# Performance work log

Hardware: AMD Instinct MI355X
Metric: run time of the kernel (lower is better)

## Reference

```python
import jax, jax.numpy as jnp
import numpy as np

WIN = 7                      # window_size[0] == window_size[1]
N_TOK = WIN * WIN            # 49 tokens per window
PRETRAIN = 12                # pretrain_window_size
LOG8 = float(np.log(8.0))


def _relative_position_index():
    # tf.meshgrid default 'xy' indexing == np.meshgrid default
    gh, gw = np.meshgrid(np.arange(WIN), np.arange(WIN))
    coords = np.stack([gh, gw], 0).reshape(2, -1)            # [2, N]
    rel = coords[:, :, None] - coords[:, None, :]            # [2, N, N]
    rel = rel.transpose(1, 2, 0)                             # [N, N, 2]
    ry = (rel[..., 0] + WIN - 1) * (2 * WIN - 1)
    rx = rel[..., 1] + WIN - 1
    return jnp.asarray((ry + rx).reshape(-1), dtype=jnp.int32)   # [N*N]


def _relative_coords_table():
    ch = np.arange(-(WIN - 1), WIN, dtype=np.float32)
    gh, gw = np.meshgrid(ch, ch)                             # 'xy' indexing
    t = np.stack([gh, gw], axis=-1)[None]                    # [1, 2W-1, 2W-1, 2]
    t = t / (PRETRAIN - 1)                                   # first divide
    t = t * (8.0 / (PRETRAIN - 1))                           # scale (as in source)
    t = np.sign(t) * np.log1p(np.abs(t)) / LOG8
    return jnp.asarray(t, dtype=jnp.float32)


REL_IDX = _relative_position_index()
COORDS_TABLE = _relative_coords_table()


def _l2_normalize(t, eps=1e-12):
    return t * jax.lax.rsqrt(jnp.maximum(jnp.sum(t * t, axis=-1, keepdims=True), eps))


def setup_inputs() -> dict:
    key = jax.random.key(0)
    ks = jax.random.split(key, 12)
    Bw, N, C, H, RPE_H = 2048, N_TOK, 512, 16, 512
    s = 0.02
    return {
        "x": jax.random.normal(ks[0], (Bw, N, C), jnp.float32),
        "mask": jax.random.normal(ks[1], (64, N, N), jnp.float32),
        "qkv_w": jax.random.normal(ks[2], (C, 3 * C), jnp.float32) * s,
        "q_bias": jnp.zeros((C,), jnp.float32),
        "v_bias": jnp.zeros((C,), jnp.float32),
        "logit_scale": jnp.full((H, 1, 1), np.log(10.0), jnp.float32),
        "rpe_w1": jax.random.normal(ks[3], (2, RPE_H), jnp.float32) * s,
        "rpe_b1": jnp.zeros((RPE_H,), jnp.float32),
        "rpe_w2": jax.random.normal(ks[4], (RPE_H, H), jnp.float32) * s,
        "proj_w": jax.random.normal(ks[5], (C, C), jnp.float32) * s,
        "proj_b": jnp.zeros((C,), jnp.float32),
    }


def reference(x, mask, qkv_w, q_bias, v_bias, logit_scale,
              rpe_w1, rpe_b1, rpe_w2, proj_w, proj_b):
    Bw, N, C = x.shape
    H = logit_scale.shape[0]
    hd = C // H

    qkv_bias = jnp.concatenate([q_bias, jnp.zeros_like(v_bias), v_bias])
    qkv = x @ qkv_w + qkv_bias                          # [Bw, N, 3C]
    qkv = qkv.reshape(Bw, N, 3, H, hd).transpose(2, 0, 3, 1, 4)
    q, k, v = qkv[0], qkv[1], qkv[2]                    # [Bw, H, N, hd]

    scale = jnp.exp(jnp.minimum(logit_scale, jnp.log(1.0 / 0.01)))  # [H,1,1]
    q = _l2_normalize(q)
    k = _l2_normalize(k)
    attn = jnp.einsum('bhnd,bhmd->bhnm', q, k) * scale  # [Bw, H, N, N]

    # RPE MLP on the (2W-1)^2 coords table, then gather per token pair
    h1 = jax.nn.relu(COORDS_TABLE @ rpe_w1 + rpe_b1)
    bias_table = (h1 @ rpe_w2).reshape(-1, H)           # [(2W-1)^2, H]
    pb = bias_table[REL_IDX].reshape(N, N, H).transpose(2, 0, 1)  # [H, N, N]
    attn = attn + 16.0 * jax.nn.sigmoid(pb)[None]

    nW = mask.shape[0]
    attn = attn.reshape(Bw // nW, nW, H, N, N) + mask[None, :, None]
    attn = attn.reshape(Bw, H, N, N)

    attn = jax.nn.softmax(attn, axis=-1)
    out = jnp.einsum('bhnm,bhmd->bnhd', attn, v).reshape(Bw, N, C)
    return out @ proj_w + proj_b
```

## Files before the change

### kernel.cpp

```cpp
#include <hip/hip_runtime.h>
#include <cstdint>

#define NTOK 49
#define CDIM 512
#define BW 2048
#define MROWS (BW * NTOK)
#define QKVN 1536

typedef __attribute__((ext_vector_type(4))) float f32x4;
typedef __attribute__((ext_vector_type(8))) short s16x8;
typedef __attribute__((ext_vector_type(4))) unsigned int u32x4;
typedef __attribute__((ext_vector_type(2))) unsigned int u32x2;

__device__ __forceinline__ uint16_t f2b(float f) {
  uint32_t u = __float_as_uint(f);
  u += 0x7fffu + ((u >> 16) & 1u);
  return (uint16_t)(u >> 16);
}
__device__ __forceinline__ float b2f(uint16_t h) {
  return __uint_as_float(((uint32_t)h) << 16);
}

#define GLOAD_LDS16(gp, lp)                                                    \
  __builtin_amdgcn_global_load_lds(                                            \
      (__attribute__((address_space(1))) void*)(gp),                           \
      (__attribute__((address_space(3))) void*)(lp), 16, 0, 0)

__global__ __launch_bounds__(256) void cvt_x_kernel(const float* __restrict__ x,
                                                    uint16_t* __restrict__ xb) {
  long i = ((long)blockIdx.x * 256 + threadIdx.x) * 4;
  f32x4 v = *(const f32x4*)(x + i);
  uint64_t p = (uint64_t)f2b(v[0]) | ((uint64_t)f2b(v[1]) << 16) |
               ((uint64_t)f2b(v[2]) << 32) | ((uint64_t)f2b(v[3]) << 48);
  *(uint64_t*)(xb + i) = p;
}

__global__ __launch_bounds__(256) void prep_weights(
    const float* __restrict__ qkv_w, const float* __restrict__ proj_w,
    const float* __restrict__ q_bias, const float* __restrict__ v_bias,
    uint16_t* __restrict__ qkv_wT, uint16_t* __restrict__ proj_wT,
    float* __restrict__ qkv_bias) {
  int i = blockIdx.x * 256 + threadIdx.x;
  if (i < QKVN * CDIM) {
    int nn = i / CDIM, kk = i % CDIM;
    qkv_wT[i] = f2b(qkv_w[(long)kk * QKVN + nn]);
  }
  if (i < CDIM * CDIM) {
    int nn = i / CDIM, kk = i % CDIM;
    proj_wT[i] = f2b(proj_w[(long)kk * CDIM + nn]);
  }
  if (i < QKVN) {
    float bv = (i < 512) ? q_bias[i] : (i < 1024 ? 0.f : v_bias[i - 1024]);
    qkv_bias[i] = bv;
  }
}

__global__ __launch_bounds__(256) void rpe_table(const float* __restrict__ w1,
                                                 const float* __restrict__ b1,
                                                 const float* __restrict__ w2,
                                                 float* __restrict__ bias16) {
  int i = blockIdx.x * 256 + threadIdx.x;
  if (i >= 169 * 16) return;
  int f = i >> 4, h = i & 15;
  float d0 = (float)((f % 13) - 6);
  float d1 = (float)((f / 13) - 6);
  const float inv_log8 = 0.4808983469629878f;
  float v0 = (d0 / 11.0f) * (8.0f / 11.0f);
  float v1 = (d1 / 11.0f) * (8.0f / 11.0f);
  float f0 = copysignf(log1pf(fabsf(v0)) * inv_log8, v0);
  if (v0 == 0.f) f0 = 0.f;
  float f1 = copysignf(log1pf(fabsf(v1)) * inv_log8, v1);
  if (v1 == 0.f) f1 = 0.f;
  float acc = 0.f;
  for (int k = 0; k < 512; ++k) {
    float h1 = fmaxf(f0 * w1[k] + f1 * w1[512 + k] + b1[k], 0.f);
    acc += h1 * w2[k * 16 + h];
  }
  bias16[i] = 16.f / (1.f + expf(-acc));
}

__global__ __launch_bounds__(256) void build_tiles(
    const float* __restrict__ mask, const float* __restrict__ bias16,
    float* __restrict__ mask_t, float* __restrict__ bias_t) {
  int bid = blockIdx.x;
  int l = threadIdx.x >> 2, j = threadIdx.x & 3;
  int gg = l >> 4, cc = l & 15;
  if (bid < 1024) {
    int w = bid >> 4, tile = bid & 15;
    int mt = tile >> 2, nt = tile & 3;
    int q = nt * 16 + cc, k = mt * 16 + gg * 4 + j;
    float v;
    if (k >= 49) v = -1e30f;
    else if (q >= 49) v = 0.f;
    else v = mask[(long)w * 2401 + q * 49 + k];
    mask_t[(long)bid * 256 + threadIdx.x] = v;
  } else {
    int idx = bid - 1024;
    int h = idx >> 4, tile = idx & 15;
    int mt = tile >> 2, nt = tile & 3;
    int q = nt * 16 + cc, k = mt * 16 + gg * 4 + j;
    float v = 0.f;
    if (q < 49 && k < 49) {
      int ridx = (q % 7 - k % 7 + 6) * 13 + (q / 7 - k / 7 + 6);
      v = bias16[ridx * 16 + h];
    }
    bias_t[(long)idx * 256 + threadIdx.x] = v;
  }
}


#define STAGE_A(tile, half, buf)                                               \
  {                                                                            \
    const uint16_t* s_ = srcA + (half) * (128L * 512) + (long)(tile) * 64;     \
    uint16_t* d_ = &lds[(buf) * 32768 + (half) * 8192 + tid * 8];              \
    GLOAD_LDS16(s_, d_);                                                       \
    GLOAD_LDS16(s_ + 64 * 512, d_ + 4096);                                     \
  }

#define STAGE_B(tile, half, buf)                                               \
  {                                                                            \
    const uint16_t* s_ = srcB + (half) * (128L * 512) + (long)(tile) * 64;     \
    uint16_t* d_ = &lds[(buf) * 32768 + 16384 + (half) * 8192 + tid * 8];      \
    GLOAD_LDS16(s_, d_);                                                       \
    GLOAD_LDS16(s_ + 64 * 512, d_ + 4096);                                     \
  }

#define VM4 asm volatile("s_waitcnt vmcnt(4)" ::: "memory");
#define VM0 asm volatile("s_waitcnt vmcnt(0)" ::: "memory");

#define PHASE(buf, q, STAGES, TAIL)                                            \
  {                                                                            \
    s16x8 a00 = *(const s16x8*)&lds[(buf)*32768 + arow + (2*(q))*1024 + ax0];  \
    s16x8 a01 = *(const s16x8*)&lds[(buf)*32768 + arow + (2*(q))*1024 + ax1];  \
    s16x8 a10 = *(const s16x8*)&lds[(buf)*32768 + arow + (2*(q)+1)*1024 + ax0];\
    s16x8 a11 = *(const s16x8*)&lds[(buf)*32768 + arow + (2*(q)+1)*1024 + ax1];\
    if ((q) == 0) {                                                            \
      _Pragma("unroll")                                                        \
      for (int nf = 0; nf < 4; ++nf) {                                         \
        bfr0[nf] = *(const s16x8*)&lds[(buf)*32768 + brow_ + nf*1024 + ax0];   \
        bfr1[nf] = *(const s16x8*)&lds[(buf)*32768 + brow_ + nf*1024 + ax1];   \
      }                                                                        \
    }                                                                          \
    STAGES                                                                     \
    __builtin_amdgcn_s_barrier();                                              \
    asm volatile("s_waitcnt lgkmcnt(0)" ::: "memory");                         \
    __builtin_amdgcn_sched_barrier(0);                                         \
    __builtin_amdgcn_s_setprio(1);                                             \
    _Pragma("unroll")                                                          \
    for (int nf = 0; nf < 4; ++nf) {                                           \
      acc[2*(q)][nf] = __builtin_amdgcn_mfma_f32_16x16x32_bf16(                \
          a00, bfr0[nf], acc[2*(q)][nf], 0, 0, 0);                             \
      acc[2*(q)][nf] = __builtin_amdgcn_mfma_f32_16x16x32_bf16(                \
          a01, bfr1[nf], acc[2*(q)][nf], 0, 0, 0);                             \
      acc[2*(q)+1][nf] = __builtin_amdgcn_mfma_f32_16x16x32_bf16(              \
          a10, bfr0[nf], acc[2*(q)+1][nf], 0, 0, 0);                           \
      acc[2*(q)+1][nf] = __builtin_amdgcn_mfma_f32_16x16x32_bf16(              \
          a11, bfr1[nf], acc[2*(q)+1][nf], 0, 0, 0);                           \
    }                                                                          \
    __builtin_amdgcn_s_setprio(0);                                             \
    TAIL                                                                       \
    __builtin_amdgcn_s_barrier();                                              \
  }

template <int EPI>
__global__ __launch_bounds__(512, 2) void gemm8p(const uint16_t* __restrict__ A,
                                                 const uint16_t* __restrict__ BT,
                                                 const float* __restrict__ bias,
                                                 void* __restrict__ Cout,
                                                 int N, int ntn) {
  __shared__ uint16_t lds[2 * 32768];
  const int tid = threadIdx.x;
  const int wave = tid >> 6, lane = tid & 63;
  const int wm = wave >> 2, wn = wave & 3;
  const int c = lane & 15, g = lane >> 4;

  const int bid = blockIdx.x;
  const int nwg = gridDim.x;
  const int wg = (bid & 7) * (nwg >> 3) + (bid >> 3);
  const int mt = wg / ntn, nt = wg % ntn;
  const long brow = (long)mt * 256;
  const int bcol = nt * 256;

  const int lr0 = tid >> 3;
  const int chunk = tid & 7;
  const int scol = (chunk ^ (lr0 & 7)) * 8;
  const uint16_t* srcA = A + (brow + lr0) * 512 + scol;
  const uint16_t* srcB = BT + ((long)bcol + lr0) * 512 + scol;

  const int arow = wm * 8192 + c * 64;
  const int brow_ = 16384 + (wn >> 1) * 8192 + ((wn & 1) * 64 + c) * 64;
  const int ax0 = (g * 8) ^ ((c & 7) * 8);
  const int ax1 = (32 + g * 8) ^ ((c & 7) * 8);

  f32x4 acc[8][4];
#pragma unroll
  for (int i = 0; i < 8; ++i)
#pragma unroll
    for (int j = 0; j < 4; ++j) acc[i][j] = f32x4{0.f, 0.f, 0.f, 0.f};
  s16x8 bfr0[4], bfr1[4];

  STAGE_A(0, 0, 0); STAGE_A(0, 1, 0);
  STAGE_B(0, 0, 0); STAGE_B(0, 1, 0);
  STAGE_B(1, 0, 1); STAGE_B(1, 1, 1);
  asm volatile("s_waitcnt vmcnt(4)" ::: "memory");
  __builtin_amdgcn_s_barrier();

  for (int i = 0; i < 3; ++i) {
    const int t0 = 2 * i;
    PHASE(0, 0, STAGE_A(t0 + 1, 0, 1), )
    PHASE(0, 1, STAGE_A(t0 + 1, 1, 1), )
    PHASE(0, 2, STAGE_B(t0 + 2, 0, 0), )
    PHASE(0, 3, STAGE_B(t0 + 2, 1, 0), VM4)
    PHASE(1, 0, STAGE_A(t0 + 2, 0, 0), )
    PHASE(1, 1, STAGE_A(t0 + 2, 1, 0), )
    PHASE(1, 2, STAGE_B(t0 + 3, 0, 1), )
    PHASE(1, 3, STAGE_B(t0 + 3, 1, 1), VM4)
  }
  PHASE(0, 0, STAGE_A(7, 0, 1), )
  PHASE(0, 1, STAGE_A(7, 1, 1), )
  PHASE(0, 2, , )
  PHASE(0, 3, , VM0)
  PHASE(1, 0, , )
  PHASE(1, 1, , )
  PHASE(1, 2, , )
  PHASE(1, 3, , )

#pragma unroll
  for (int mf = 0; mf < 8; ++mf) {
#pragma unroll
    for (int nf = 0; nf < 4; ++nf) {
      const int col = bcol + wn * 64 + nf * 16 + c;
      const float bv = bias[col];
#pragma unroll
      for (int r = 0; r < 4; ++r) {
        const long grow = brow + wm * 128 + mf * 16 + g * 4 + r;
        const float v = acc[mf][nf][r] + bv;
        if (EPI == 0)
          ((uint16_t*)Cout)[grow * N + col] = f2b(v);
        else
          ((float*)Cout)[grow * N + col] = v;
      }
    }
  }
}

__global__ __launch_bounds__(256, 4) void attn_mfma(
    const uint16_t* __restrict__ qkv,
    const float* __restrict__ logit_scale,
    const float* __restrict__ bias_t,
    const float* __restrict__ mask_t,
    uint16_t* __restrict__ outb) {
  __shared__ uint16_t Vs[4][2048];
  const int tid = threadIdx.x;
  const int wave = tid >> 6, lane = tid & 63;
  const int g = lane >> 4, c = lane & 15;
  const int b = blockIdx.x >> 2;
  const int h = ((blockIdx.x & 3) << 2) | wave;
  const long rbase = (long)b * 49;

  uint16_t* vdst = Vs[wave];
#pragma unroll
  for (int i = 0; i < 4; ++i) {
    int chunk = i * 64 + lane;
    int row = chunk >> 2, part = chunk & 3;
    if (row > 48) { row = 0; part = 0; }
    GLOAD_LDS16(qkv + (rbase + row) * QKVN + 1024 + h * 32 + part * 8,
                vdst + i * 512 + lane * 8);
  }

  const long qoff = rbase * QKVN + h * 32;
  s16x8 kf[4], qf[4];
#pragma unroll
  for (int t = 0; t < 4; ++t) {
    int row = t * 16 + c;
    s16x8 kv = {}, qv = {};
    if (row < 49) {
      qv = *(const s16x8*)(qkv + qoff + (long)row * QKVN + g * 8);
      kv = *(const s16x8*)(qkv + qoff + (long)row * QKVN + 512 + g * 8);
    }
    float kfv[8], qfv[8];
    float kss = 0.f, qss = 0.f;
#pragma unroll
    for (int m = 0; m < 8; ++m) {
      kfv[m] = b2f((uint16_t)kv[m]); kss += kfv[m] * kfv[m];
      qfv[m] = b2f((uint16_t)qv[m]); qss += qfv[m] * qfv[m];
    }
    kss += __shfl_xor(kss, 16); kss += __shfl_xor(kss, 32);
    qss += __shfl_xor(qss, 16); qss += __shfl_xor(qss, 32);
    float kr = rsqrtf(fmaxf(kss, 1e-12f));
    float qr = rsqrtf(fmaxf(qss, 1e-12f));
#pragma unroll
    for (int m = 0; m < 8; ++m) {
      kv[m] = (short)f2b(kfv[m] * kr);
      qv[m] = (short)f2b(qfv[m] * qr);
    }
    kf[t] = kv; qf[t] = qv;
  }

  const float scale = __expf(fminf(logit_scale[h], 4.6051702f));
  const float* bt = bias_t + (long)h * 4096;
  const float* mk = mask_t + (long)(b & 63) * 4096;

  u32x4 aT[4][2];
  const int dstlo = (c + 16 * (g >> 1)) * 4;
  const int dsthi = (c + 16 * (2 + (g >> 1))) * 4;
  const bool godd = (g & 1) != 0;
  const bool low = (lane < 32);

#pragma unroll
  for (int nt = 0; nt < 4; ++nt) {
    f32x4 eb[4], em[4];
#pragma unroll
    for (int mt = 0; mt < 4; ++mt) {
      int tile = mt * 4 + nt;
      eb[mt] = *(const f32x4*)(bt + tile * 256 + lane * 4);
      em[mt] = *(const f32x4*)(mk + tile * 256 + lane * 4);
    }
    f32x4 sv[4];
    __builtin_amdgcn_s_setprio(1);
#pragma unroll
    for (int mt = 0; mt < 4; ++mt)
      sv[mt] = __builtin_amdgcn_mfma_f32_16x16x32_bf16(
          kf[mt], qf[nt], f32x4{0.f, 0.f, 0.f, 0.f}, 0, 0, 0);
    __builtin_amdgcn_s_setprio(0);
#pragma unroll
    for (int mt = 0; mt < 4; ++mt)
#pragma unroll
      for (int j = 0; j < 4; ++j)
        sv[mt][j] = sv[mt][j] * scale + eb[mt][j] + em[mt][j];

    float mx = -3.0e38f;
#pragma unroll
    for (int mt = 0; mt < 4; ++mt)
#pragma unroll
      for (int j = 0; j < 4; ++j) mx = fmaxf(mx, sv[mt][j]);
    mx = fmaxf(mx, __shfl_xor(mx, 16));
    mx = fmaxf(mx, __shfl_xor(mx, 32));
    float sum = 0.f;
#pragma unroll
    for (int mt = 0; mt < 4; ++mt)
#pragma unroll
      for (int j = 0; j < 4; ++j) {
        float e = __expf(sv[mt][j] - mx);
        sv[mt][j] = e; sum += e;
      }
    sum += __shfl_xor(sum, 16);
    sum += __shfl_xor(sum, 32);
    float inv = 1.0f / sum;
#pragma unroll
    for (int mt = 0; mt < 4; ++mt)
#pragma unroll
      for (int j = 0; j < 4; ++j) sv[mt][j] *= inv;

    unsigned pk[4][2];
#pragma unroll
    for (int mt = 0; mt < 4; ++mt) {
      pk[mt][0] = (unsigned)f2b(sv[mt][0]) | ((unsigned)f2b(sv[mt][1]) << 16);
      pk[mt][1] = (unsigned)f2b(sv[mt][2]) | ((unsigned)f2b(sv[mt][3]) << 16);
    }
#pragma unroll
    for (int x = 0; x < 2; ++x)
#pragma unroll
      for (int K = 0; K < 2; ++K) {
        int vA = godd ? (int)pk[2 * K + 1][x] : (int)pk[2 * K][x];
        int dA = godd ? dsthi : dstlo;
        int rA = __builtin_amdgcn_ds_permute(dA, vA);
        int vB = godd ? (int)pk[2 * K][x] : (int)pk[2 * K + 1][x];
        int dB = godd ? dstlo : dsthi;
        int rB = __builtin_amdgcn_ds_permute(dB, vB);
        aT[nt][K][x]     = (unsigned)(low ? rA : rB);
        aT[nt][K][2 + x] = (unsigned)(low ? rB : rA);
      }
  }

  asm volatile("s_waitcnt vmcnt(0)" ::: "memory");

  f32x4 o[4][2];
#pragma unroll
  for (int qt = 0; qt < 4; ++qt)
#pragma unroll
    for (int dt = 0; dt < 2; ++dt) o[qt][dt] = f32x4{0.f, 0.f, 0.f, 0.f};

#pragma unroll
  for (int ks = 0; ks < 2; ++ks) {
    s16x8 vf[2];
#pragma unroll
    for (int dt = 0; dt < 2; ++dt) {
      int d = dt * 16 + c;
      s16x8 vv;
#pragma unroll
      for (int jj = 0; jj < 8; ++jj) {
        int k = ks * 32 + g * 8 + jj;
        vv[jj] = (short)vdst[k * 32 + d];
      }
      vf[dt] = vv;
    }
    __builtin_amdgcn_s_setprio(1);
#pragma unroll
    for (int qt = 0; qt < 4; ++qt) {
      s16x8 pf = __builtin_bit_cast(s16x8, aT[qt][ks]);
#pragma unroll
      for (int dt = 0; dt < 2; ++dt)
        o[qt][dt] = __builtin_amdgcn_mfma_f32_16x16x32_bf16(pf, vf[dt],
                                                            o[qt][dt], 0, 0, 0);
    }
    __builtin_amdgcn_s_setprio(0);
  }

#pragma unroll
  for (int qt = 0; qt < 4; ++qt) {
    int q0 = qt * 16 + g * 4;
#pragma unroll
    for (int dt = 0; dt < 2; ++dt) {
      int d = dt * 16 + c;
#pragma unroll
      for (int j = 0; j < 4; ++j) {
        int q = q0 + j;
        if (q < 49)
          outb[(rbase + q) * 512 + h * 32 + d] = f2b(o[qt][dt][j]);
      }
    }
  }
}

extern "C" void kernel_launch(void* const* d_in, const int* in_sizes, int n_in,
                              void* d_out, int out_size, void* d_ws,
                              size_t ws_size, hipStream_t stream) {
  const float* x = (const float*)d_in[0];
  const float* mask = (const float*)d_in[1];
  const float* qkv_w = (const float*)d_in[2];
  const float* q_bias = (const float*)d_in[3];
  const float* v_bias = (const float*)d_in[4];
  const float* logit_scale = (const float*)d_in[5];
  const float* rpe_w1 = (const float*)d_in[6];
  const float* rpe_b1 = (const float*)d_in[7];
  const float* rpe_w2 = (const float*)d_in[8];
  const float* proj_w = (const float*)d_in[9];
  const float* proj_b = (const float*)d_in[10];

  char* ws = (char*)d_ws;
  uint16_t* xb       = (uint16_t*)ws;
  uint16_t* qkvbuf   = (uint16_t*)(ws + 102760448L);
  uint16_t* qkv_wT   = (uint16_t*)(ws + 411041792L);
  uint16_t* proj_wT  = (uint16_t*)(ws + 412614656L);
  float*    qkv_bias = (float*)(ws + 413138944L);
  float*    bias16   = (float*)(ws + 413145088L);
  float*    bias_t   = (float*)(ws + 413155904L);
  float*    mask_t   = (float*)(ws + 413418048L);

  cvt_x_kernel<<<50176, 256, 0, stream>>>(x, xb);
  prep_weights<<<3072, 256, 0, stream>>>(qkv_w, proj_w, q_bias, v_bias, qkv_wT,
                                         proj_wT, qkv_bias);
  rpe_table<<<11, 256, 0, stream>>>(rpe_w1, rpe_b1, rpe_w2, bias16);
  build_tiles<<<1280, 256, 0, stream>>>(mask, bias16, mask_t, bias_t);

  gemm8p<0><<<2352, 512, 0, stream>>>(xb, qkv_wT, qkv_bias, qkvbuf, QKVN, 6);
  attn_mfma<<<8192, 256, 0, stream>>>(qkvbuf, logit_scale, bias_t, mask_t, xb);
  gemm8p<1><<<784, 512, 0, stream>>>(xb, proj_wT, proj_b, d_out, CDIM, 2);
}
```

Before: 562.0 us.

## Fuse prep kernels and interleave PV MFMA with software-pipelined bias loads

Merges the x conversion, weight transpose and RPE table kernels into a single launch, which removes two kernel launches. In the attention kernel, V fragments are loaded up front and the PV MFMAs run inside the per-query-tile loop, so the full transposed probability array no longer has to stay live. Bias and mask tiles for the next query tile are prefetched while the current one is processed. Separately, the QKV GEMM is split into two half-sized launches, which adds launch overhead without an obvious gain, and the extra prefetch registers may offset the register savings.

```diff
diff --git a/kernel.cpp b/kernel.cpp
--- a/kernel.cpp
+++ b/kernel.cpp
@@ -26,57 +26,55 @@
       (__attribute__((address_space(1))) void*)(gp),                           \
       (__attribute__((address_space(3))) void*)(lp), 16, 0, 0)
 
-__global__ __launch_bounds__(256) void cvt_x_kernel(const float* __restrict__ x,
-                                                    uint16_t* __restrict__ xb) {
-  long i = ((long)blockIdx.x * 256 + threadIdx.x) * 4;
-  f32x4 v = *(const f32x4*)(x + i);
-  uint64_t p = (uint64_t)f2b(v[0]) | ((uint64_t)f2b(v[1]) << 16) |
-               ((uint64_t)f2b(v[2]) << 32) | ((uint64_t)f2b(v[3]) << 48);
-  *(uint64_t*)(xb + i) = p;
-}
-
-__global__ __launch_bounds__(256) void prep_weights(
+__global__ __launch_bounds__(256) void prep_all(
+    const float* __restrict__ x, uint16_t* __restrict__ xb,
     const float* __restrict__ qkv_w, const float* __restrict__ proj_w,
     const float* __restrict__ q_bias, const float* __restrict__ v_bias,
     uint16_t* __restrict__ qkv_wT, uint16_t* __restrict__ proj_wT,
-    float* __restrict__ qkv_bias) {
-  int i = blockIdx.x * 256 + threadIdx.x;
-  if (i < QKVN * CDIM) {
-    int nn = i / CDIM, kk = i % CDIM;
-    qkv_wT[i] = f2b(qkv_w[(long)kk * QKVN + nn]);
-  }
-  if (i < CDIM * CDIM) {
-    int nn = i / CDIM, kk = i % CDIM;
-    proj_wT[i] = f2b(proj_w[(long)kk * CDIM + nn]);
-  }
-  if (i < QKVN) {
-    float bv = (i < 512) ? q_bias[i] : (i < 1024 ? 0.f : v_bias[i - 1024]);
-    qkv_bias[i] = bv;
-  }
-}
-
-__global__ __launch_bounds__(256) void rpe_table(const float* __restrict__ w1,
-                                                 const float* __restrict__ b1,
-                                                 const float* __restrict__ w2,
-                                                 float* __restrict__ bias16) {
-  int i = blockIdx.x * 256 + threadIdx.x;
-  if (i >= 169 * 16) return;
-  int f = i >> 4, h = i & 15;
-  float d0 = (float)((f % 13) - 6);
-  float d1 = (float)((f / 13) - 6);
-  const float inv_log8 = 0.4808983469629878f;
-  float v0 = (d0 / 11.0f) * (8.0f / 11.0f);
-  float v1 = (d1 / 11.0f) * (8.0f / 11.0f);
-  float f0 = copysignf(log1pf(fabsf(v0)) * inv_log8, v0);
-  if (v0 == 0.f) f0 = 0.f;
-  float f1 = copysignf(log1pf(fabsf(v1)) * inv_log8, v1);
-  if (v1 == 0.f) f1 = 0.f;
-  float acc = 0.f;
-  for (int k = 0; k < 512; ++k) {
-    float h1 = fmaxf(f0 * w1[k] + f1 * w1[512 + k] + b1[k], 0.f);
-    acc += h1 * w2[k * 16 + h];
-  }
-  bias16[i] = 16.f / (1.f + expf(-acc));
+    float* __restrict__ qkv_bias, const float* __restrict__ w1,
+    const float* __restrict__ b1, const float* __restrict__ w2,
+    float* __restrict__ bias16) {
+  const int bid = blockIdx.x;
+  if (bid < 50176) {
+    long i = ((long)bid * 256 + threadIdx.x) * 4;
+    f32x4 v = *(const f32x4*)(x + i);
+    uint64_t p = (uint64_t)f2b(v[0]) | ((uint64_t)f2b(v[1]) << 16) |
+                 ((uint64_t)f2b(v[2]) << 32) | ((uint64_t)f2b(v[3]) << 48);
+    *(uint64_t*)(xb + i) = p;
+  } else if (bid < 50176 + 3072) {
+    int i = (bid - 50176) * 256 + threadIdx.x;
+    if (i < QKVN * CDIM) {
+      int nn = i / CDIM, kk = i % CDIM;
+      qkv_wT[i] = f2b(qkv_w[(long)kk * QKVN + nn]);
+    }
+    if (i < CDIM * CDIM) {
+      int nn = i / CDIM, kk = i % CDIM;
+      proj_wT[i] = f2b(proj_w[(long)kk * CDIM + nn]);
+    }
+    if (i < QKVN) {
+      float bv = (i < 512) ? q_bias[i] : (i < 1024 ? 0.f : v_bias[i - 1024]);
+      qkv_bias[i] = bv;
+    }
+  } else {
+    int i = (bid - 53248) * 256 + threadIdx.x;
+    if (i >= 169 * 16) return;
+    int f = i >> 4, h = i & 15;
+    float d0 = (float)((f % 13) - 6);
+    float d1 = (float)((f / 13) - 6);
+    const float inv_log8 = 0.4808983469629878f;
+    float v0 = (d0 / 11.0f) * (8.0f / 11.0f);
+    float v1 = (d1 / 11.0f) * (8.0f / 11.0f);
+    float f0 = copysignf(log1pf(fabsf(v0)) * inv_log8, v0);
+    if (v0 == 0.f) f0 = 0.f;
+    float f1 = copysignf(log1pf(fabsf(v1)) * inv_log8, v1);
+    if (v1 == 0.f) f1 = 0.f;
+    float acc = 0.f;
+    for (int k = 0; k < 512; ++k) {
+      float h1 = fmaxf(f0 * w1[k] + f1 * w1[512 + k] + b1[k], 0.f);
+      acc += h1 * w2[k * 16 + h];
+    }
+    bias16[i] = 16.f / (1.f + expf(-acc));
+  }
 }
 
 __global__ __launch_bounds__(256) void build_tiles(
@@ -297,25 +295,46 @@
     kf[t] = kv; qf[t] = qv;
   }
 
+  asm volatile("s_waitcnt vmcnt(0)" ::: "memory");
+  s16x8 vf[2][2];
+#pragma unroll
+  for (int ks = 0; ks < 2; ++ks)
+#pragma unroll
+    for (int dt = 0; dt < 2; ++dt) {
+      int d = dt * 16 + c;
+      s16x8 vv;
+#pragma unroll
+      for (int jj = 0; jj < 8; ++jj) {
+        int k = ks * 32 + g * 8 + jj;
+        vv[jj] = (short)vdst[k * 32 + d];
+      }
+      vf[ks][dt] = vv;
+    }
+
   const float scale = __expf(fminf(logit_scale[h], 4.6051702f));
   const float* bt = bias_t + (long)h * 4096;
   const float* mk = mask_t + (long)(b & 63) * 4096;
 
-  u32x4 aT[4][2];
   const int dstlo = (c + 16 * (g >> 1)) * 4;
   const int dsthi = (c + 16 * (2 + (g >> 1))) * 4;
   const bool godd = (g & 1) != 0;
   const bool low = (lane < 32);
 
+  f32x4 cbA[4], cmA[4];
+#pragma unroll
+  for (int mt = 0; mt < 4; ++mt) {
+    cbA[mt] = *(const f32x4*)(bt + (mt * 4 + 0) * 256 + lane * 4);
+    cmA[mt] = *(const f32x4*)(mk + (mt * 4 + 0) * 256 + lane * 4);
+  }
+
+  f32x4 o[4][2];
+#pragma unroll
+  for (int qt = 0; qt < 4; ++qt)
+#pragma unroll
+    for (int dt = 0; dt < 2; ++dt) o[qt][dt] = f32x4{0.f, 0.f, 0.f, 0.f};
+
 #pragma unroll
   for (int nt = 0; nt < 4; ++nt) {
-    f32x4 eb[4], em[4];
-#pragma unroll
-    for (int mt = 0; mt < 4; ++mt) {
-      int tile = mt * 4 + nt;
-      eb[mt] = *(const f32x4*)(bt + tile * 256 + lane * 4);
-      em[mt] = *(const f32x4*)(mk + tile * 256 + lane * 4);
-    }
     f32x4 sv[4];
     __builtin_amdgcn_s_setprio(1);
 #pragma unroll
@@ -323,11 +342,21 @@
       sv[mt] = __builtin_amdgcn_mfma_f32_16x16x32_bf16(
           kf[mt], qf[nt], f32x4{0.f, 0.f, 0.f, 0.f}, 0, 0, 0);
     __builtin_amdgcn_s_setprio(0);
+
+    f32x4 cbN[4], cmN[4];
+    if (nt < 3) {
+#pragma unroll
+      for (int mt = 0; mt < 4; ++mt) {
+        cbN[mt] = *(const f32x4*)(bt + (mt * 4 + nt + 1) * 256 + lane * 4);
+        cmN[mt] = *(const f32x4*)(mk + (mt * 4 + nt + 1) * 256 + lane * 4);
+      }
+    }
+
 #pragma unroll
     for (int mt = 0; mt < 4; ++mt)
 #pragma unroll
       for (int j = 0; j < 4; ++j)
-        sv[mt][j] = sv[mt][j] * scale + eb[mt][j] + em[mt][j];
+        sv[mt][j] = sv[mt][j] * scale + cbA[mt][j] + cmA[mt][j];
 
     float mx = -3.0e38f;
 #pragma unroll
@@ -358,6 +387,7 @@
       pk[mt][0] = (unsigned)f2b(sv[mt][0]) | ((unsigned)f2b(sv[mt][1]) << 16);
       pk[mt][1] = (unsigned)f2b(sv[mt][2]) | ((unsigned)f2b(sv[mt][3]) << 16);
     }
+    u32x4 aT2[2];
 #pragma unroll
     for (int x = 0; x < 2; ++x)
 #pragma unroll
@@ -368,43 +398,25 @@
         int vB = godd ? (int)pk[2 * K][x] : (int)pk[2 * K + 1][x];
         int dB = godd ? dstlo : dsthi;
         int rB = __builtin_amdgcn_ds_permute(dB, vB);
-        aT[nt][K][x]     = (unsigned)(low ? rA : rB);
-        aT[nt][K][2 + x] = (unsigned)(low ? rB : rA);
-      }
-  }
-
-  asm volatile("s_waitcnt vmcnt(0)" ::: "memory");
-
-  f32x4 o[4][2];
-#pragma unroll
-  for (int qt = 0; qt < 4; ++qt)
-#pragma unroll
-    for (int dt = 0; dt < 2; ++dt) o[qt][dt] = f32x4{0.f, 0.f, 0.f, 0.f};
-
-#pragma unroll
-  for (int ks = 0; ks < 2; ++ks) {
-    s16x8 vf[2];
-#pragma unroll
-    for (int dt = 0; dt < 2; ++dt) {
-      int d = dt * 16 + c;
-      s16x8 vv;
-#pragma unroll
-      for (int jj = 0; jj < 8; ++jj) {
-        int k = ks * 32 + g * 8 + jj;
-        vv[jj] = (short)vdst[k * 32 + d];
-      }
-      vf[dt] = vv;
-    }
+        aT2[K][x]     = (unsigned)(low ? rA : rB);
+        aT2[K][2 + x] = (unsigned)(low ? rB : rA);
+      }
+
     __builtin_amdgcn_s_setprio(1);
 #pragma unroll
-    for (int qt = 0; qt < 4; ++qt) {
-      s16x8 pf = __builtin_bit_cast(s16x8, aT[qt][ks]);
+    for (int ks = 0; ks < 2; ++ks) {
+      s16x8 pf = __builtin_bit_cast(s16x8, aT2[ks]);
 #pragma unroll
       for (int dt = 0; dt < 2; ++dt)
-        o[qt][dt] = __builtin_amdgcn_mfma_f32_16x16x32_bf16(pf, vf[dt],
-                                                            o[qt][dt], 0, 0, 0);
+        o[nt][dt] = __builtin_amdgcn_mfma_f32_16x16x32_bf16(pf, vf[ks][dt],
+                                                            o[nt][dt], 0, 0, 0);
     }
     __builtin_amdgcn_s_setprio(0);
+
+    if (nt < 3) {
+#pragma unroll
+      for (int mt = 0; mt < 4; ++mt) { cbA[mt] = cbN[mt]; cmA[mt] = cmN[mt]; }
+    }
   }
 
 #pragma unroll
@@ -448,13 +460,14 @@
   float*    bias_t   = (float*)(ws + 413155904L);
   float*    mask_t   = (float*)(ws + 413418048L);
 
-  cvt_x_kernel<<<50176, 256, 0, stream>>>(x, xb);
-  prep_weights<<<3072, 256, 0, stream>>>(qkv_w, proj_w, q_bias, v_bias, qkv_wT,
-                                         proj_wT, qkv_bias);
-  rpe_table<<<11, 256, 0, stream>>>(rpe_w1, rpe_b1, rpe_w2, bias16);
+  prep_all<<<53259, 256, 0, stream>>>(x, xb, qkv_w, proj_w, q_bias, v_bias,
+                                      qkv_wT, proj_wT, qkv_bias, rpe_w1,
+                                      rpe_b1, rpe_w2, bias16);
   build_tiles<<<1280, 256, 0, stream>>>(mask, bias16, mask_t, bias_t);
 
-  gemm8p<0><<<2352, 512, 0, stream>>>(xb, qkv_wT, qkv_bias, qkvbuf, QKVN, 6);
+  gemm8p<0><<<1176, 512, 0, stream>>>(xb, qkv_wT, qkv_bias, qkvbuf, QKVN, 6);
+  gemm8p<0><<<1176, 512, 0, stream>>>(xb + 25690112L, qkv_wT, qkv_bias,
+                                      qkvbuf + 77070336L, QKVN, 6);
   attn_mfma<<<8192, 256, 0, stream>>>(qkvbuf, logit_scale, bias_t, mask_t, xb);
   gemm8p<1><<<784, 512, 0, stream>>>(xb, proj_wT, proj_b, d_out, CDIM, 2);
 }
```

Result: slower. 625.7 us (+11.4%).
